# Kernel tuning notes

Measured on AMD Instinct MI355X. Metric: run time of the kernel, lower is better.

## Reference

```python
import jax, jax.numpy as jnp
import numpy as np

N_NODES = 100000
N_EDGES = 1600000
IN_C, HID_C, OUT_C = 64, 128, 64


def _sage_conv(x, src, dst, Wl, bl, Wr, n_nodes):
    # PyG SAGEConv (mean aggr): out = lin_l(mean_{j in N(i)} x_j) + lin_r(x_i)
    msg = x[src]  # [E, C] gather
    agg = jax.ops.segment_sum(msg, dst, num_segments=n_nodes)
    deg = jax.ops.segment_sum(jnp.ones((src.shape[0],), x.dtype), dst, num_segments=n_nodes)
    agg = agg / jnp.maximum(deg, 1.0)[:, None]
    return agg @ Wl + bl + x @ Wr


def setup_inputs() -> dict:
    key = jax.random.key(0)
    ks = jax.random.split(key, 16)
    x = jax.random.normal(ks[0], (N_NODES, IN_C), dtype=jnp.float32)
    edge_index = jax.random.randint(ks[1], (2, N_EDGES), 0, N_NODES, dtype=jnp.int64)
    s = 0.05
    return {
        "x": x,
        "edge_index": edge_index,
        # conv1: SAGEConv(IN_C, HID_C)
        "Wl1": jax.random.normal(ks[2], (IN_C, HID_C), jnp.float32) * s,
        "bl1": jnp.zeros((HID_C,), jnp.float32),
        "Wr1": jax.random.normal(ks[3], (IN_C, HID_C), jnp.float32) * s,
        # conv2: SAGEConv(HID_C, OUT_C)
        "Wl2": jax.random.normal(ks[4], (HID_C, OUT_C), jnp.float32) * s,
        "bl2": jnp.zeros((OUT_C,), jnp.float32),
        "Wr2": jax.random.normal(ks[5], (HID_C, OUT_C), jnp.float32) * s,
        # classifier MLP: OUT_C -> HID_C -> HID_C//2 -> 1
        "Wc1": jax.random.normal(ks[6], (OUT_C, HID_C), jnp.float32) * s,
        "bc1": jnp.zeros((HID_C,), jnp.float32),
        "Wc2": jax.random.normal(ks[7], (HID_C, HID_C // 2), jnp.float32) * s,
        "bc2": jnp.zeros((HID_C // 2,), jnp.float32),
        "Wc3": jax.random.normal(ks[8], (HID_C // 2, 1), jnp.float32) * s,
        "bc3": jnp.zeros((1,), jnp.float32),
    }


def reference(x, edge_index, Wl1, bl1, Wr1, Wl2, bl2, Wr2, Wc1, bc1, Wc2, bc2, Wc3, bc3):
    src, dst = edge_index[0], edge_index[1]
    n = x.shape[0]
    h = _sage_conv(x, src, dst, Wl1, bl1, Wr1, n)
    h = jax.nn.relu(h)  # dropout is identity in eval mode
    embeddings = _sage_conv(h, src, dst, Wl2, bl2, Wr2, n)
    # classifier head
    c = jax.nn.relu(embeddings @ Wc1 + bc1)
    c = jax.nn.relu(c @ Wc2 + bc2)
    fraud_probs = jax.nn.sigmoid(c @ Wc3 + bc3)
    return embeddings, fraud_probs
```

## Files before the change

### kernel.cpp

```cpp
#include <hip/hip_runtime.h>
#include <math.h>

#define N_NODES 100000
#define ZERO_NODE 100000
#define N_EDGES 1600000
#define NBKT    391
#define BCAP    5120
#define EPB     4096
#define NBLKA   391
#define PADBKT  1792
#define BUCKET_CAP (N_EDGES + NBKT * PADBKT)

using short8  = __attribute__((ext_vector_type(8))) short;
using float4v = __attribute__((ext_vector_type(4))) float;

__device__ inline unsigned short f2bf(float f) {
    unsigned int u = __float_as_uint(f);
    u += 0x7fffu + ((u >> 16) & 1u);
    return (unsigned short)(u >> 16);
}
__device__ inline float bflo(unsigned int v) { return __uint_as_float(v << 16); }
__device__ inline float bfhi(unsigned int v) { return __uint_as_float(v & 0xffff0000u); }

__global__ void prep_all(const float* __restrict__ x, unsigned short* __restrict__ xb,
                         const float* __restrict__ Wl1, const float* __restrict__ Wr1,
                         const float* __restrict__ Wl2, const float* __restrict__ Wr2,
                         const float* __restrict__ Wc1, const float* __restrict__ Wc2,
                         unsigned short* __restrict__ w1, unsigned short* __restrict__ w2,
                         unsigned short* __restrict__ wcls1, unsigned short* __restrict__ wcls2,
                         unsigned short* __restrict__ t2b) {
    int bid = blockIdx.x;
    int t = threadIdx.x;
    if (bid < 6250) {
        int i = bid * 256 + t;
        float4 v = *(const float4*)(x + (long)i * 4);
        uint2 o;
        o.x = (unsigned)f2bf(v.x) | ((unsigned)f2bf(v.y) << 16);
        o.y = (unsigned)f2bf(v.z) | ((unsigned)f2bf(v.w) << 16);
        *(uint2*)(xb + (long)i * 4) = o;
    } else if (bid < 6442) {
        int i = (bid - 6250) * 256 + t;
        if (i < 16384) {
            int n = i >> 7, k = i & 127;
            float v = (k < 64) ? Wl1[k * 128 + n] : Wr1[(k - 64) * 128 + n];
            w1[i] = f2bf(v);
        } else if (i < 32768) {
            int j = i - 16384; int n = j >> 7, k = j & 127;
            float v = (n < 64) ? Wl2[k * 64 + n] : Wr2[k * 64 + (n - 64)];
            w2[j] = f2bf(v);
        } else if (i < 40960) {
            int j = i - 32768; int n = j >> 6, k = j & 63;
            wcls1[j] = f2bf(Wc1[k * 128 + n]);
        } else {
            int j = i - 40960; int n = j >> 7, k = j & 127;
            wcls2[j] = f2bf(Wc2[k * 64 + n]);
        }
    } else {
        if (t < 32)       ((unsigned*)(xb  + (long)ZERO_NODE * 64))[t]      = 0u;
        else if (t < 64)  ((unsigned*)(t2b + (long)ZERO_NODE * 64))[t - 32] = 0u;
    }
}

__global__ __launch_bounds__(256) void binA(const int* __restrict__ esrc,
                                            const int* __restrict__ edst,
                                            int* __restrict__ bcnt,
                                            unsigned* __restrict__ stage) {
    __shared__ int hist[NBKT];
    __shared__ int rbase[NBKT];
    int t = threadIdx.x;
    for (int i = t; i < NBKT; i += 256) hist[i] = 0;
    __syncthreads();
    int e0 = blockIdx.x * EPB;
    int e1 = e0 + EPB; if (e1 > N_EDGES) e1 = N_EDGES;
    unsigned pk[16];
    int bn[16];
#pragma unroll
    for (int j = 0; j < 16; j++) {
        int e = e0 + j * 256 + t;
        bn[j] = -1;
        if (e < N_EDGES && e < e1) {
            int d = edst[e];
            int s = esrc[e];
            int b = d >> 8;
            pk[j] = (unsigned)s | ((unsigned)(d & 255) << 24);
            bn[j] = b;
            atomicAdd(&hist[b], 1);
        }
    }
    __syncthreads();
    for (int i = t; i < NBKT; i += 256) {
        int c = hist[i];
        rbase[i] = c ? atomicAdd(&bcnt[i], c) : 0;
        hist[i] = 0;
    }
    __syncthreads();
#pragma unroll
    for (int j = 0; j < 16; j++) {
        if (bn[j] >= 0) {
            int b = bn[j];
            int slot = rbase[b] + atomicAdd(&hist[b], 1);
            if (slot < BCAP)
                stage[(long)b * BCAP + slot] = pk[j];
        }
    }
}

__global__ void binScan(const int* __restrict__ bcnt, int* __restrict__ pbase) {
    __shared__ int s[512];
    int t = threadIdx.x;
    int v = (t < NBKT) ? bcnt[t] : 0;
    s[t] = v;
    __syncthreads();
    for (int st = 1; st < 512; st <<= 1) {
        int a = (t >= st) ? s[t - st] : 0;
        __syncthreads();
        s[t] += a;
        __syncthreads();
    }
    if (t < NBKT) pbase[t] = (s[t] - v) + t * PADBKT;
}

__global__ __launch_bounds__(256) void binB(const int* __restrict__ bcnt,
                                            const int* __restrict__ pbase,
                                            const unsigned* __restrict__ stage,
                                            int* __restrict__ offp, int* __restrict__ deg,
                                            int* __restrict__ bucket) {
    __shared__ int hist[256];
    __shared__ int scn[256];
    __shared__ int lbase[256];
    int b = blockIdx.x, t = threadIdx.x;
    int cnt = bcnt[b];
    if (cnt > BCAP) cnt = BCAP;
    int base = pbase[b];
    hist[t] = 0;
    __syncthreads();
    const unsigned* sp = stage + (long)b * BCAP;
    unsigned pk[20];
    int nv = 0;
#pragma unroll
    for (int j = 0; j < 20; j++) {
        int i = j * 256 + t;
        if (i < cnt) {
            pk[j] = sp[i];
            atomicAdd(&hist[pk[j] >> 24], 1);
            nv = j + 1;
        }
    }
    __syncthreads();
    int v = hist[t];
    int p8 = (v + 7) & ~7;
    scn[t] = p8;
    __syncthreads();
    for (int st = 1; st < 256; st <<= 1) {
        int a = (t >= st) ? scn[t - st] : 0;
        __syncthreads();
        scn[t] += a;
        __syncthreads();
    }
    lbase[t] = scn[t] - p8;
    int node = b * 256 + t;
    if (node < N_NODES) {
        offp[node] = base + lbase[t];
        deg[node]  = v;
    }
    hist[t] = 0;
    __syncthreads();
#pragma unroll
    for (int j = 0; j < 20; j++) {
        if (j < nv) {
            unsigned p = pk[j];
            int ln = p >> 24;
            int slot = atomicAdd(&hist[ln], 1);
            bucket[base + lbase[ln] + slot] = (int)(p & 0xFFFFFFu);
        }
    }
    int ps = base + lbase[t] + v;
    int pe = base + lbase[t] + p8;
    for (int j = ps; j < pe; j++) bucket[j] = ZERO_NODE;
}

__global__ __launch_bounds__(256, 8) void gather_b(
        const unsigned short* __restrict__ y, const int* __restrict__ offp,
        const int* __restrict__ deg, const int* __restrict__ bucket,
        unsigned short* __restrict__ outb) {
    int node = __builtin_amdgcn_readfirstlane(blockIdx.x * 4 + (threadIdx.x >> 6));
    int lane = threadIdx.x & 63;
    int g = lane >> 3, c8 = lane & 7;
    int e0 = offp[node];
    int dg = deg[node];
    int e1p = e0 + ((dg + 7) & ~7);
    const char* yb = (const char*)y;
    float a[8] = {0.f, 0.f, 0.f, 0.f, 0.f, 0.f, 0.f, 0.f};
    for (int base = e0; base < e1p; base += 32) {
        uint4 v[4];
#pragma unroll
        for (int h = 0; h < 4; h++) {
            if (base + h * 8 < e1p) {
                int s = bucket[base + h * 8 + g];
                unsigned off32 = ((unsigned)s << 7) + ((unsigned)c8 << 4);
                v[h] = *(const uint4*)(yb + off32);
            } else {
                v[h] = (uint4){0u, 0u, 0u, 0u};
            }
        }
#pragma unroll
        for (int h = 0; h < 4; h++) {
            a[0] += bflo(v[h].x); a[1] += bfhi(v[h].x);
            a[2] += bflo(v[h].y); a[3] += bfhi(v[h].y);
            a[4] += bflo(v[h].z); a[5] += bfhi(v[h].z);
            a[6] += bflo(v[h].w); a[7] += bfhi(v[h].w);
        }
    }
#pragma unroll
    for (int j = 0; j < 8; j++) {
        a[j] += __shfl_xor(a[j], 8);
        a[j] += __shfl_xor(a[j], 16);
        a[j] += __shfl_xor(a[j], 32);
    }
    if (g == 0) {
        float sc = 1.f / fmaxf((float)dg, 1.f);
        uint4 o;
        o.x = (unsigned)f2bf(a[0]*sc) | ((unsigned)f2bf(a[1]*sc) << 16);
        o.y = (unsigned)f2bf(a[2]*sc) | ((unsigned)f2bf(a[3]*sc) << 16);
        o.z = (unsigned)f2bf(a[4]*sc) | ((unsigned)f2bf(a[5]*sc) << 16);
        o.w = (unsigned)f2bf(a[6]*sc) | ((unsigned)f2bf(a[7]*sc) << 16);
        *(uint4*)(outb + (long)node * 64 + c8 * 8) = o;
    }
}

__global__ __launch_bounds__(256, 8) void gather_badd(
        const unsigned short* __restrict__ y, const int* __restrict__ offp,
        const int* __restrict__ deg, const int* __restrict__ bucket,
        const float* __restrict__ add, float* __restrict__ out) {
    int node = __builtin_amdgcn_readfirstlane(blockIdx.x * 4 + (threadIdx.x >> 6));
    int lane = threadIdx.x & 63;
    int g = lane >> 3, c8 = lane & 7;
    int e0 = offp[node];
    int dg = deg[node];
    int e1p = e0 + ((dg + 7) & ~7);
    const char* yb = (const char*)y;
    float a[8] = {0.f, 0.f, 0.f, 0.f, 0.f, 0.f, 0.f, 0.f};
    for (int base = e0; base < e1p; base += 32) {
        uint4 v[4];
#pragma unroll
        for (int h = 0; h < 4; h++) {
            if (base + h * 8 < e1p) {
                int s = bucket[base + h * 8 + g];
                unsigned off32 = ((unsigned)s << 7) + ((unsigned)c8 << 4);
                v[h] = *(const uint4*)(yb + off32);
            } else {
                v[h] = (uint4){0u, 0u, 0u, 0u};
            }
        }
#pragma unroll
        for (int h = 0; h < 4; h++) {
            a[0] += bflo(v[h].x); a[1] += bfhi(v[h].x);
            a[2] += bflo(v[h].y); a[3] += bfhi(v[h].y);
            a[4] += bflo(v[h].z); a[5] += bfhi(v[h].z);
            a[6] += bflo(v[h].w); a[7] += bfhi(v[h].w);
        }
    }
#pragma unroll
    for (int j = 0; j < 8; j++) {
        a[j] += __shfl_xor(a[j], 8);
        a[j] += __shfl_xor(a[j], 16);
        a[j] += __shfl_xor(a[j], 32);
    }
    if (g == 0) {
        float sc = 1.f / fmaxf((float)dg, 1.f);
        const float4* up = (const float4*)(add + (long)node * 64 + c8 * 8);
        float4 u0 = up[0], u1 = up[1];
        float4 r0 = { a[0]*sc + u0.x, a[1]*sc + u0.y, a[2]*sc + u0.z, a[3]*sc + u0.w };
        float4 r1 = { a[4]*sc + u1.x, a[5]*sc + u1.y, a[6]*sc + u1.z, a[7]*sc + u1.w };
        float4* op = (float4*)(out + (long)node * 64 + c8 * 8);
        op[0] = r0; op[1] = r1;
    }
}

__global__ __launch_bounds__(256, 4) void fused_conv(
        const unsigned short* __restrict__ xb, const unsigned short* __restrict__ aggb,
        const unsigned short* __restrict__ w1, const float* __restrict__ bl1,
        const unsigned short* __restrict__ w2, const float* __restrict__ bl2,
        unsigned short* __restrict__ t2b, float* __restrict__ u) {
    __shared__ __align__(16) unsigned short smemA[64 * 136];
    __shared__ __align__(16) unsigned short smemH[64 * 136];
    unsigned short* sA = smemA;
    unsigned short* sH = smemH;
    float* su = (float*)smemA;
    unsigned short* st2 = smemH;

    int t = threadIdx.x;
    int lane = t & 63;
    int wv = t >> 6;
    int q = lane >> 4, ln = lane & 15;

    long base = (long)blockIdx.x * 4096;
    long maxe = (long)N_NODES * 64 - 8;
#pragma unroll
    for (int it = 0; it < 2; it++) {
        int i = it * 256 + t;
        int m = i >> 3, k8 = (i & 7) * 8;
        long g = base + (long)m * 64 + k8;
        if (g > maxe) g = maxe;
        *(uint4*)(sA + m * 136 + k8)      = *(const uint4*)(aggb + g);
        *(uint4*)(sA + m * 136 + 64 + k8) = *(const uint4*)(xb + g);
    }
    __syncthreads();

    int n0 = wv * 32;
    float4v acc[2][4];
    {
        float b0 = bl1[n0 + ln], b1 = bl1[n0 + 16 + ln];
#pragma unroll
        for (int mi = 0; mi < 4; mi++) {
            acc[0][mi] = (float4v){b0, b0, b0, b0};
            acc[1][mi] = (float4v){b1, b1, b1, b1};
        }
    }
#pragma unroll
    for (int ks = 0; ks < 4; ks++) {
        int k0 = ks * 32 + q * 8;
        short8 bf0 = *(const short8*)(w1 + (long)(n0 + ln) * 128 + k0);
        short8 bf1 = *(const short8*)(w1 + (long)(n0 + 16 + ln) * 128 + k0);
#pragma unroll
        for (int mi = 0; mi < 4; mi++) {
            short8 af = *(const short8*)(sA + (mi * 16 + ln) * 136 + k0);
            acc[0][mi] = __builtin_amdgcn_mfma_f32_16x16x32_bf16(af, bf0, acc[0][mi], 0, 0, 0);
            acc[1][mi] = __builtin_amdgcn_mfma_f32_16x16x32_bf16(af, bf1, acc[1][mi], 0, 0, 0);
        }
    }
#pragma unroll
    for (int j = 0; j < 2; j++)
#pragma unroll
        for (int mi = 0; mi < 4; mi++) {
            int n = n0 + j * 16 + ln;
#pragma unroll
            for (int r = 0; r < 4; r++) {
                int m = mi * 16 + q * 4 + r;
                sH[m * 136 + n] = f2bf(fmaxf(acc[j][mi][r], 0.f));
            }
        }
    __syncthreads();

    float4v acc2[2][4];
    {
        float c0 = (n0 >= 64) ? bl2[n0 - 64 + ln] : 0.f;
        float c1 = (n0 >= 64) ? bl2[n0 - 48 + ln] : 0.f;
#pragma unroll
        for (int mi = 0; mi < 4; mi++) {
            acc2[0][mi] = (float4v){c0, c0, c0, c0};
            acc2[1][mi] = (float4v){c1, c1, c1, c1};
        }
    }
#pragma unroll
    for (int ks = 0; ks < 4; ks++) {
        int k0 = ks * 32 + q * 8;
        short8 bf0 = *(const short8*)(w2 + (long)(n0 + ln) * 128 + k0);
        short8 bf1 = *(const short8*)(w2 + (long)(n0 + 16 + ln) * 128 + k0);
#pragma unroll
        for (int mi = 0; mi < 4; mi++) {
            short8 af = *(const short8*)(sH + (mi * 16 + ln) * 136 + k0);
            acc2[0][mi] = __builtin_amdgcn_mfma_f32_16x16x32_bf16(af, bf0, acc2[0][mi], 0, 0, 0);
            acc2[1][mi] = __builtin_amdgcn_mfma_f32_16x16x32_bf16(af, bf1, acc2[1][mi], 0, 0, 0);
        }
    }
    __syncthreads();

#pragma unroll
    for (int j = 0; j < 2; j++)
#pragma unroll
        for (int mi = 0; mi < 4; mi++) {
            int n = n0 + j * 16 + ln;
#pragma unroll
            for (int r = 0; r < 4; r++) {
                int m = mi * 16 + q * 4 + r;
                if (wv < 2) st2[m * 72 + n] = f2bf(acc2[j][mi][r]);
                else        su[m * 68 + (n - 64)] = acc2[j][mi][r];
            }
        }
    __syncthreads();

    long lim = (long)N_NODES * 64;
    unsigned int* t2u = (unsigned int*)(t2b + base);
#pragma unroll
    for (int it = 0; it < 8; it++) {
        int i = it * 256 + t;
        long g = base + (long)i * 2;
        if (g + 1 < lim) {
            int m = (i * 2) >> 6, n = (i * 2) & 63;
            t2u[i] = (unsigned)st2[m * 72 + n] | ((unsigned)st2[m * 72 + n + 1] << 16);
        }
    }
#pragma unroll
    for (int it = 0; it < 16; it++) {
        int i = it * 256 + t;
        long g = base + i;
        if (g < lim) u[g] = su[(i >> 6) * 68 + (i & 63)];
    }
}

__global__ __launch_bounds__(256, 4) void fused_cls(
        const float* __restrict__ emb,
        const unsigned short* __restrict__ wcls1, const float* __restrict__ bc1,
        const unsigned short* __restrict__ wcls2, const float* __restrict__ bc2,
        const float* __restrict__ wc3, const float* __restrict__ bc3,
        float* __restrict__ probs) {
    __shared__ __align__(16) unsigned short smem[64 * 136];
    __shared__ float psum[4][64];
    unsigned short* sE = smem;
    unsigned short* sC = smem;

    int t = threadIdx.x;
    int wv = t >> 6;
    int lane = t & 63;
    int q = lane >> 4, ln = lane & 15;

    long base = (long)blockIdx.x * 4096;
    long maxe = (long)N_NODES * 64 - 4;
#pragma unroll
    for (int it = 0; it < 4; it++) {
        int i = it * 256 + t;
        int m = i >> 4, k4 = (i & 15) * 4;
        long g = base + (long)m * 64 + k4;
        if (g > maxe) g = maxe;
        float4 v = *(const float4*)(emb + g);
        uint2 o;
        o.x = (unsigned)f2bf(v.x) | ((unsigned)f2bf(v.y) << 16);
        o.y = (unsigned)f2bf(v.z) | ((unsigned)f2bf(v.w) << 16);
        *(uint2*)(sE + m * 72 + k4) = o;
    }
    __syncthreads();

    int n0 = wv * 32;
    float4v acc[2][4];
    {
        float b0 = bc1[n0 + ln], b1 = bc1[n0 + 16 + ln];
#pragma unroll
        for (int mi = 0; mi < 4; mi++) {
            acc[0][mi] = (float4v){b0, b0, b0, b0};
            acc[1][mi] = (float4v){b1, b1, b1, b1};
        }
    }
#pragma unroll
    for (int ks = 0; ks < 2; ks++) {
        int k0 = ks * 32 + q * 8;
        short8 bf0 = *(const short8*)(wcls1 + (long)(n0 + ln) * 64 + k0);
        short8 bf1 = *(const short8*)(wcls1 + (long)(n0 + 16 + ln) * 64 + k0);
#pragma unroll
        for (int mi = 0; mi < 4; mi++) {
            short8 af = *(const short8*)(sE + (mi * 16 + ln) * 72 + k0);
            acc[0][mi] = __builtin_amdgcn_mfma_f32_16x16x32_bf16(af, bf0, acc[0][mi], 0, 0, 0);
            acc[1][mi] = __builtin_amdgcn_mfma_f32_16x16x32_bf16(af, bf1, acc[1][mi], 0, 0, 0);
        }
    }
    __syncthreads();
#pragma unroll
    for (int j = 0; j < 2; j++)
#pragma unroll
        for (int mi = 0; mi < 4; mi++) {
            int n = n0 + j * 16 + ln;
#pragma unroll
            for (int r = 0; r < 4; r++) {
                int m = mi * 16 + q * 4 + r;
                sC[m * 136 + n] = f2bf(fmaxf(acc[j][mi][r], 0.f));
            }
        }
    __syncthreads();

    int n0c = wv * 16;
    float4v acc3[4];
    {
        float b = bc2[n0c + ln];
#pragma unroll
        for (int mi = 0; mi < 4; mi++) acc3[mi] = (float4v){b, b, b, b};
    }
#pragma unroll
    for (int ks = 0; ks < 4; ks++) {
        int k0 = ks * 32 + q * 8;
        short8 bf0 = *(const short8*)(wcls2 + (long)(n0c + ln) * 128 + k0);
#pragma unroll
        for (int mi = 0; mi < 4; mi++) {
            short8 af = *(const short8*)(sC + (mi * 16 + ln) * 136 + k0);
            acc3[mi] = __builtin_amdgcn_mfma_f32_16x16x32_bf16(af, bf0, acc3[mi], 0, 0, 0);
        }
    }
    float w3 = wc3[n0c + ln];
#pragma unroll
    for (int mi = 0; mi < 4; mi++)
#pragma unroll
        for (int r = 0; r < 4; r++) {
            float v = fmaxf(acc3[mi][r], 0.f) * w3;
            v += __shfl_xor(v, 1);
            v += __shfl_xor(v, 2);
            v += __shfl_xor(v, 4);
            v += __shfl_xor(v, 8);
            if (ln == 0) psum[wv][mi * 16 + q * 4 + r] = v;
        }
    __syncthreads();
    if (t < 64) {
        int node = blockIdx.x * 64 + t;
        if (node < N_NODES) {
            float tot = psum[0][t] + psum[1][t] + psum[2][t] + psum[3][t] + bc3[0];
            probs[node] = 1.f / (1.f + expf(-tot));
        }
    }
}

extern "C" void kernel_launch(void* const* d_in, const int* in_sizes, int n_in,
                              void* d_out, int out_size, void* d_ws, size_t ws_size,
                              hipStream_t stream) {
    const float* x   = (const float*)d_in[0];
    const int*   ei  = (const int*)d_in[1];
    const float* Wl1 = (const float*)d_in[2];
    const float* bl1 = (const float*)d_in[3];
    const float* Wr1 = (const float*)d_in[4];
    const float* Wl2 = (const float*)d_in[5];
    const float* bl2 = (const float*)d_in[6];
    const float* Wr2 = (const float*)d_in[7];
    const float* Wc1 = (const float*)d_in[8];
    const float* bc1 = (const float*)d_in[9];
    const float* Wc2 = (const float*)d_in[10];
    const float* bc2 = (const float*)d_in[11];
    const float* Wc3 = (const float*)d_in[12];
    const float* bc3 = (const float*)d_in[13];

    float* out = (float*)d_out;

    int* iw     = (int*)d_ws;
    int* bcnt   = iw;
    int* pbase  = iw + 512;
    int* offp   = iw + 1024;
    int* deg    = iw + 1024 + 100352;
    int* bucket = iw + 1024 + 2 * 100352;
    unsigned* stage = (unsigned*)(bucket + BUCKET_CAP);
    size_t ioff = ((size_t)(1024 + 2 * 100352 + BUCKET_CAP) + (size_t)NBKT * BCAP) * 4;
    ioff = (ioff + 127) & ~(size_t)127;

    char* wsb = (char*)d_ws;
    unsigned short* xb    = (unsigned short*)(wsb + ioff);
    unsigned short* agg1b = xb + 6400064L;
    unsigned short* t2b   = agg1b + 6400000L;
    float*          u     = (float*)(t2b + 6400064L);
    unsigned short* w1    = (unsigned short*)(u + 6400000L);
    unsigned short* w2    = w1 + 16384;
    unsigned short* wcls1 = w2 + 16384;
    unsigned short* wcls2 = wcls1 + 8192;

    float* emb   = out;
    float* probs = out + 6400000L;

    const int* esrc = ei;
    const int* edst = ei + N_EDGES;

    hipMemsetAsync(bcnt, 0, 1024 * sizeof(int), stream);

    prep_all<<<6443, 256, 0, stream>>>(x, xb, Wl1, Wr1, Wl2, Wr2, Wc1, Wc2,
                                       w1, w2, wcls1, wcls2, t2b);

    binA<<<NBLKA, 256, 0, stream>>>(esrc, edst, bcnt, stage);
    binScan<<<1, 512, 0, stream>>>(bcnt, pbase);
    binB<<<NBKT, 256, 0, stream>>>(bcnt, pbase, stage, offp, deg, bucket);

    gather_b<<<25000, 256, 0, stream>>>(xb, offp, deg, bucket, agg1b);
    fused_conv<<<1563, 256, 0, stream>>>(xb, agg1b, w1, bl1, w2, bl2, t2b, u);
    gather_badd<<<25000, 256, 0, stream>>>(t2b, offp, deg, bucket, u, emb);
    fused_cls<<<1563, 256, 0, stream>>>(emb, wcls1, bc1, wcls2, bc2, Wc3, bc3, probs);
}
```

Measured before the change: 269.8 us.

## Pack two nodes per wavefront in gathers, pad buckets to 4, store u in bf16

The gather kernels now process two nodes per 64-lane wavefront, each half using 4 edge groups, so a block covers 8 nodes. Buckets are padded to multiples of 4 instead of 8, which cuts dummy-edge loads for low-degree nodes. Out-of-range lanes redirect to the zero node rather than taking a branch. The root-term intermediate u is stored as bf16 instead of fp32, halving its write and read traffic at some precision cost. Reads can now run past a bucket end, so the bucket capacity gains a BCAP tail.

```diff
diff --git a/kernel.cpp b/kernel.cpp
--- a/kernel.cpp
+++ b/kernel.cpp
@@ -8,8 +8,8 @@
 #define BCAP    5120
 #define EPB     4096
 #define NBLKA   391
-#define PADBKT  1792
-#define BUCKET_CAP (N_EDGES + NBKT * PADBKT)
+#define PADBKT  768
+#define BUCKET_CAP (N_EDGES + NBKT * PADBKT + BCAP)
 
 using short8  = __attribute__((ext_vector_type(8))) short;
 using float4v = __attribute__((ext_vector_type(4))) float;
@@ -148,8 +148,8 @@
     }
     __syncthreads();
     int v = hist[t];
-    int p8 = (v + 7) & ~7;
-    scn[t] = p8;
+    int p4 = (v + 3) & ~3;
+    scn[t] = p4;
     __syncthreads();
     for (int st = 1; st < 256; st <<= 1) {
         int a = (t >= st) ? scn[t - st] : 0;
@@ -157,7 +157,7 @@
         scn[t] += a;
         __syncthreads();
     }
-    lbase[t] = scn[t] - p8;
+    lbase[t] = scn[t] - p4;
     int node = b * 256 + t;
     if (node < N_NODES) {
         offp[node] = base + lbase[t];
@@ -175,7 +175,7 @@
         }
     }
     int ps = base + lbase[t] + v;
-    int pe = base + lbase[t] + p8;
+    int pe = base + lbase[t] + p4;
     for (int j = ps; j < pe; j++) bucket[j] = ZERO_NODE;
 }
 
@@ -183,25 +183,27 @@
         const unsigned short* __restrict__ y, const int* __restrict__ offp,
         const int* __restrict__ deg, const int* __restrict__ bucket,
         unsigned short* __restrict__ outb) {
-    int node = __builtin_amdgcn_readfirstlane(blockIdx.x * 4 + (threadIdx.x >> 6));
-    int lane = threadIdx.x & 63;
-    int g = lane >> 3, c8 = lane & 7;
+    int t = threadIdx.x;
+    int wv = t >> 6, lane = t & 63;
+    int nh = lane >> 5;
+    int g  = (lane >> 3) & 3;
+    int c8 = lane & 7;
+    int node = blockIdx.x * 8 + wv * 2 + nh;
     int e0 = offp[node];
     int dg = deg[node];
-    int e1p = e0 + ((dg + 7) & ~7);
+    int len = (dg + 3) & ~3;
+    int maxlen = max(len, __shfl_xor(len, 32));
     const char* yb = (const char*)y;
     float a[8] = {0.f, 0.f, 0.f, 0.f, 0.f, 0.f, 0.f, 0.f};
-    for (int base = e0; base < e1p; base += 32) {
+    for (int base = 0; base < maxlen; base += 16) {
         uint4 v[4];
 #pragma unroll
         for (int h = 0; h < 4; h++) {
-            if (base + h * 8 < e1p) {
-                int s = bucket[base + h * 8 + g];
-                unsigned off32 = ((unsigned)s << 7) + ((unsigned)c8 << 4);
-                v[h] = *(const uint4*)(yb + off32);
-            } else {
-                v[h] = (uint4){0u, 0u, 0u, 0u};
-            }
+            int rel = base + h * 4 + g;
+            int s = bucket[e0 + rel];
+            s = (rel < len) ? s : ZERO_NODE;
+            unsigned off32 = ((unsigned)s << 7) + ((unsigned)c8 << 4);
+            v[h] = *(const uint4*)(yb + off32);
         }
 #pragma unroll
         for (int h = 0; h < 4; h++) {
@@ -215,7 +217,6 @@
     for (int j = 0; j < 8; j++) {
         a[j] += __shfl_xor(a[j], 8);
         a[j] += __shfl_xor(a[j], 16);
-        a[j] += __shfl_xor(a[j], 32);
     }
     if (g == 0) {
         float sc = 1.f / fmaxf((float)dg, 1.f);
@@ -231,26 +232,28 @@
 __global__ __launch_bounds__(256, 8) void gather_badd(
         const unsigned short* __restrict__ y, const int* __restrict__ offp,
         const int* __restrict__ deg, const int* __restrict__ bucket,
-        const float* __restrict__ add, float* __restrict__ out) {
-    int node = __builtin_amdgcn_readfirstlane(blockIdx.x * 4 + (threadIdx.x >> 6));
-    int lane = threadIdx.x & 63;
-    int g = lane >> 3, c8 = lane & 7;
+        const unsigned short* __restrict__ ub, float* __restrict__ out) {
+    int t = threadIdx.x;
+    int wv = t >> 6, lane = t & 63;
+    int nh = lane >> 5;
+    int g  = (lane >> 3) & 3;
+    int c8 = lane & 7;
+    int node = blockIdx.x * 8 + wv * 2 + nh;
     int e0 = offp[node];
     int dg = deg[node];
-    int e1p = e0 + ((dg + 7) & ~7);
+    int len = (dg + 3) & ~3;
+    int maxlen = max(len, __shfl_xor(len, 32));
     const char* yb = (const char*)y;
     float a[8] = {0.f, 0.f, 0.f, 0.f, 0.f, 0.f, 0.f, 0.f};
-    for (int base = e0; base < e1p; base += 32) {
+    for (int base = 0; base < maxlen; base += 16) {
         uint4 v[4];
 #pragma unroll
         for (int h = 0; h < 4; h++) {
-            if (base + h * 8 < e1p) {
-                int s = bucket[base + h * 8 + g];
-                unsigned off32 = ((unsigned)s << 7) + ((unsigned)c8 << 4);
-                v[h] = *(const uint4*)(yb + off32);
-            } else {
-                v[h] = (uint4){0u, 0u, 0u, 0u};
-            }
+            int rel = base + h * 4 + g;
+            int s = bucket[e0 + rel];
+            s = (rel < len) ? s : ZERO_NODE;
+            unsigned off32 = ((unsigned)s << 7) + ((unsigned)c8 << 4);
+            v[h] = *(const uint4*)(yb + off32);
         }
 #pragma unroll
         for (int h = 0; h < 4; h++) {
@@ -264,14 +267,15 @@
     for (int j = 0; j < 8; j++) {
         a[j] += __shfl_xor(a[j], 8);
         a[j] += __shfl_xor(a[j], 16);
-        a[j] += __shfl_xor(a[j], 32);
     }
     if (g == 0) {
         float sc = 1.f / fmaxf((float)dg, 1.f);
-        const float4* up = (const float4*)(add + (long)node * 64 + c8 * 8);
-        float4 u0 = up[0], u1 = up[1];
-        float4 r0 = { a[0]*sc + u0.x, a[1]*sc + u0.y, a[2]*sc + u0.z, a[3]*sc + u0.w };
-        float4 r1 = { a[4]*sc + u1.x, a[5]*sc + u1.y, a[6]*sc + u1.z, a[7]*sc + u1.w };
+        uint2 uv = *(const uint2*)(ub + (long)node * 64 + c8 * 8);
+        float4 r0 = { a[0]*sc + bflo(uv.x), a[1]*sc + bfhi(uv.x),
+                      a[2]*sc + bflo(uv.y), a[3]*sc + bfhi(uv.y) };
+        uint2 uw = *(const uint2*)(ub + (long)node * 64 + c8 * 8 + 4);
+        float4 r1 = { a[4]*sc + bflo(uw.x), a[5]*sc + bfhi(uw.x),
+                      a[6]*sc + bflo(uw.y), a[7]*sc + bfhi(uw.y) };
         float4* op = (float4*)(out + (long)node * 64 + c8 * 8);
         op[0] = r0; op[1] = r1;
     }
@@ -281,12 +285,12 @@
         const unsigned short* __restrict__ xb, const unsigned short* __restrict__ aggb,
         const unsigned short* __restrict__ w1, const float* __restrict__ bl1,
         const unsigned short* __restrict__ w2, const float* __restrict__ bl2,
-        unsigned short* __restrict__ t2b, float* __restrict__ u) {
+        unsigned short* __restrict__ t2b, unsigned short* __restrict__ ub) {
     __shared__ __align__(16) unsigned short smemA[64 * 136];
     __shared__ __align__(16) unsigned short smemH[64 * 136];
     unsigned short* sA = smemA;
     unsigned short* sH = smemH;
-    float* su = (float*)smemA;
+    unsigned short* stu = smemA;
     unsigned short* st2 = smemH;
 
     int t = threadIdx.x;
@@ -375,27 +379,24 @@
             for (int r = 0; r < 4; r++) {
                 int m = mi * 16 + q * 4 + r;
                 if (wv < 2) st2[m * 72 + n] = f2bf(acc2[j][mi][r]);
-                else        su[m * 68 + (n - 64)] = acc2[j][mi][r];
+                else        stu[m * 72 + (n - 64)] = f2bf(acc2[j][mi][r]);
             }
         }
     __syncthreads();
 
-    long lim = (long)N_NODES * 64;
-    unsigned int* t2u = (unsigned int*)(t2b + base);
+    long lim2 = (long)N_NODES * 32;
+    unsigned* t2u = (unsigned*)t2b;
+    unsigned* uu  = (unsigned*)ub;
+    long ubase = base >> 1;
 #pragma unroll
     for (int it = 0; it < 8; it++) {
         int i = it * 256 + t;
-        long g = base + (long)i * 2;
-        if (g + 1 < lim) {
+        long gq = ubase + i;
+        if (gq < lim2) {
             int m = (i * 2) >> 6, n = (i * 2) & 63;
-            t2u[i] = (unsigned)st2[m * 72 + n] | ((unsigned)st2[m * 72 + n + 1] << 16);
-        }
-    }
-#pragma unroll
-    for (int it = 0; it < 16; it++) {
-        int i = it * 256 + t;
-        long g = base + i;
-        if (g < lim) u[g] = su[(i >> 6) * 68 + (i & 63)];
+            t2u[gq] = (unsigned)st2[m * 72 + n] | ((unsigned)st2[m * 72 + n + 1] << 16);
+            uu[gq]  = (unsigned)stu[m * 72 + n] | ((unsigned)stu[m * 72 + n + 1] << 16);
+        }
     }
 }
 
@@ -540,8 +541,8 @@
     unsigned short* xb    = (unsigned short*)(wsb + ioff);
     unsigned short* agg1b = xb + 6400064L;
     unsigned short* t2b   = agg1b + 6400000L;
-    float*          u     = (float*)(t2b + 6400064L);
-    unsigned short* w1    = (unsigned short*)(u + 6400000L);
+    unsigned short* ub    = t2b + 6400064L;
+    unsigned short* w1    = ub + 6400000L;
     unsigned short* w2    = w1 + 16384;
     unsigned short* wcls1 = w2 + 16384;
     unsigned short* wcls2 = wcls1 + 8192;
@@ -561,8 +562,8 @@
     binScan<<<1, 512, 0, stream>>>(bcnt, pbase);
     binB<<<NBKT, 256, 0, stream>>>(bcnt, pbase, stage, offp, deg, bucket);
 
-    gather_b<<<25000, 256, 0, stream>>>(xb, offp, deg, bucket, agg1b);
-    fused_conv<<<1563, 256, 0, stream>>>(xb, agg1b, w1, bl1, w2, bl2, t2b, u);
-    gather_badd<<<25000, 256, 0, stream>>>(t2b, offp, deg, bucket, u, emb);
+    gather_b<<<12500, 256, 0, stream>>>(xb, offp, deg, bucket, agg1b);
+    fused_conv<<<1563, 256, 0, stream>>>(xb, agg1b, w1, bl1, w2, bl2, t2b, ub);
+    gather_badd<<<12500, 256, 0, stream>>>(t2b, offp, deg, bucket, ub, emb);
     fused_cls<<<1563, 256, 0, stream>>>(emb, wcls1, bc1, wcls2, bc2, Wc3, bc3, probs);
 }
```

Result: faster. 247.8 us (-8.1%).
